# Kernel optimization log

Hardware: AMD Instinct MI355X
Metric: run time of the kernel (lower is better)

## Reference

```python
import jax, jax.numpy as jnp
import numpy as np
import math

N, L, C, H, K = 4, 16384, 256, 8, 4
D = C // H


def setup_inputs():
    rng = jax.random.key(0)
    ks = jax.random.split(rng, 16)
    def w(k, shape, scale):
        return jax.random.normal(k, shape, jnp.float32) * scale
    s = 1.0 / math.sqrt(C)
    return {
        "query": jax.random.normal(ks[0], (N, L, C), jnp.float32),
        "key": jax.random.normal(ks[1], (N, L, C), jnp.float32),
        "value": jax.random.normal(ks[2], (N, L, C), jnp.float32),
        "reference_points": jax.random.uniform(ks[3], (N, L, 2), jnp.float32),
        "pos_embed": jax.random.normal(ks[4], (N, L, C), jnp.float32),
        "Wq": w(ks[5], (C, C), s), "bq": jnp.zeros((C,), jnp.float32),
        "Wk": w(ks[6], (C, C), s), "bk": jnp.zeros((C,), jnp.float32),
        "Wv": w(ks[7], (C, C), s), "bv": jnp.zeros((C,), jnp.float32),
        "Wo1": w(ks[8], (C, 2 * C), s), "bo1": jnp.zeros((2 * C,), jnp.float32),
        "Wo2": w(ks[9], (2 * C, H * K * 2), 0.02), "bo2": w(ks[10], (H * K * 2,), 0.02),
        "Wpos": w(ks[11], (C, C), s), "bpos": jnp.zeros((C,), jnp.float32),
        "Wout": w(ks[12], (C, C), s), "bout": jnp.zeros((C,), jnp.float32),
    }


def _sample_weight(points):
    # F.grid_sample on a 1x1 feature map (bilinear, zeros padding, align_corners=False)
    # degenerates to a scalar weight: grid g = 2p-1, unnormalized c = g/2 = p - 0.5,
    # pixel-0 bilinear weight per axis = max(0, 1 - |c|).
    c = points - 0.5
    return jax.nn.relu(1.0 - jnp.abs(c[..., 0])) * jax.nn.relu(1.0 - jnp.abs(c[..., 1]))


def reference(query, key, value, reference_points, pos_embed,
              Wq, bq, Wk, bk, Wv, bv, Wo1, bo1, Wo2, bo2, Wpos, bpos, Wout, bout):
    Nb, Ln, Cd = query.shape
    q = (query @ Wq + bq).reshape(Nb, Ln, H, D)
    k = (key @ Wk + bk).reshape(Nb, Ln, H, D)
    v = (value @ Wv + bv).reshape(Nb, Ln, H, D)
    pos = (pos_embed @ Wpos + bpos).reshape(Nb, Ln, H, D)
    q = q + pos
    k = k + pos
    # offset MLP: Linear(C,2C) -> ReLU -> Linear(2C, H*K*2)
    offsets = (jax.nn.relu(query @ Wo1 + bo1) @ Wo2 + bo2).reshape(Nb, Ln, H, K, 2)
    sp = reference_points[:, :, None, None, :] + offsets  # [N,L,H,K,2]
    w = _sample_weight(sp)                                # [N,L,H,K]
    # sampled_k[n,l,h,k,:] = k[n,l,h,:] * w[n,l,h,k]  (1x1 grid_sample closed form)
    qk = jnp.einsum('nlhd,nlhd->nlh', q, k)               # [N,L,H]
    attn = jax.nn.softmax(qk[..., None] * w / math.sqrt(D), axis=-1)  # [N,L,H,K]
    # output = sum_k attn_k * (v * w_k) = v * sum_k(attn_k * w_k)
    wv = jnp.sum(attn * w, axis=-1)                       # [N,L,H]
    out = (v * wv[..., None]).reshape(Nb, Ln, Cd)
    return out @ Wout + bout
```

## Files before the change

### kernel.cpp

```cpp
#include <hip/hip_runtime.h>
#include <hip/hip_bf16.h>

typedef __bf16 bf16x8 __attribute__((ext_vector_type(8)));
typedef float f32x4 __attribute__((ext_vector_type(4)));
typedef float f32x2 __attribute__((ext_vector_type(2)));

#define MT 32
#define CC 256

__device__ __forceinline__ int swz(int r, int c) {
    return r * 512 + ((c * 2) ^ ((r & 7) << 4));
}
__device__ __forceinline__ int swzH(int r, int c) {
    return r * 1024 + ((c * 2) ^ ((r & 7) << 4));
}

__device__ __forceinline__ void zero4(f32x4 (&acc)[2][4]) {
#pragma unroll
    for (int i = 0; i < 2; ++i)
#pragma unroll
        for (int j = 0; j < 4; ++j)
            acc[i][j] = (f32x4){0.f, 0.f, 0.f, 0.f};
}

__device__ __forceinline__ void stage_load(const float* __restrict__ src, int row0, int tid,
                                           f32x4 (&v)[8]) {
#pragma unroll
    for (int i = 0; i < 8; ++i) {
        int f = i * 256 + tid;
        int r = f >> 6;
        int c = (f & 63) * 4;
        v[i] = __builtin_nontemporal_load((const f32x4*)(src + (size_t)(row0 + r) * CC + c));
    }
}
__device__ __forceinline__ void stage_write(__bf16* dst, int tid, const f32x4 (&v)[8]) {
#pragma unroll
    for (int i = 0; i < 8; ++i) {
        int f = i * 256 + tid;
        int r = f >> 6;
        int c = (f & 63) * 4;
        union { __bf16 h[4]; unsigned long long u; } uu;
        uu.h[0] = (__bf16)v[i][0]; uu.h[1] = (__bf16)v[i][1];
        uu.h[2] = (__bf16)v[i][2]; uu.h[3] = (__bf16)v[i][3];
        *(unsigned long long*)((char*)dst + swz(r, c)) = uu.u;
    }
}

__global__ void prep_all(const float* __restrict__ Wq, const float* __restrict__ Wk,
                         const float* __restrict__ Wpos, const float* __restrict__ Wo1,
                         const float* __restrict__ Wo2, const float* __restrict__ Wv,
                         const float* __restrict__ Wout, __bf16* __restrict__ ws)
{
    int i = blockIdx.x * 256 + threadIdx.x;
    if (i >= 557056) return;
    int j, K, N;
    const float* S0 = nullptr; const float* S1 = nullptr;
    if (i < 131072)      { j = i;          K = 512; N = 256; S0 = Wq;  S1 = Wpos; }
    else if (i < 262144) { j = i - 131072; K = 512; N = 256; S0 = Wk;  S1 = Wpos; }
    else if (i < 393216) { j = i - 262144; K = 256; N = 512; S0 = Wo1; }
    else if (i < 425984) { j = i - 393216; K = 512; N = 64;  S0 = Wo2; }
    else if (i < 491520) { j = i - 425984; K = 256; N = 256; S0 = Wv; }
    else                 { j = i - 491520; K = 256; N = 256; S0 = Wout; }
    int tile = j >> 9, r = j & 511;
    int lane = r >> 3, e = r & 7;
    int q4 = lane >> 4, r16 = lane & 15;
    int KC = K >> 5;
    int nc = tile / KC, kc = tile - nc * KC;
    int k = kc * 32 + q4 * 8 + e;
    int n = nc * 16 + r16;
    float v;
    if (S1 && k >= 256) v = S1[(size_t)(k - 256) * N + n];
    else                v = S0[(size_t)k * N + n];
    ws[i] = (__bf16)v;
}

extern "C" __global__ void __launch_bounds__(256, 2)
fused_ext_attn(const float* __restrict__ query, const float* __restrict__ key,
               const float* __restrict__ value, const float* __restrict__ refp,
               const float* __restrict__ pose,
               const __bf16* __restrict__ ws,
               const float* __restrict__ bq, const float* __restrict__ bk,
               const float* __restrict__ bv, const float* __restrict__ bpos,
               const float* __restrict__ bo1, const float* __restrict__ bo2,
               const float* __restrict__ bout,
               float* __restrict__ out)
{
    const __bf16* WTqp  = ws;
    const __bf16* WTkp  = ws + 131072;
    const __bf16* WTo1  = ws + 262144;
    const __bf16* WTo2  = ws + 393216;
    const __bf16* WTv   = ws + 425984;
    const __bf16* WTout = ws + 491520;

    __shared__ __attribute__((aligned(16))) __bf16 SA[MT * CC];
    __shared__ __attribute__((aligned(16))) __bf16 SB[MT * CC];
    __shared__ __attribute__((aligned(16))) __bf16 SC[MT * CC];
    __shared__ __attribute__((aligned(16))) char   H1[32768];

    float* off_s = (float*)H1;
    float* qk_s  = (float*)(H1 + 8192);
    float* wv_s  = (float*)(H1 + 9216);

    const int tid = threadIdx.x;
    const int lane = tid & 63;
    const int wid = tid >> 6;
    const int r16 = lane & 15;
    const int q4 = lane >> 4;
    const int laneoff = lane * 8;
    const int row0 = blockIdx.x * MT;

    f32x4 vq[8], vp[8], vkey[8];
    stage_load(query, row0, tid, vq);
    stage_load(pose, row0, tid, vp);
    stage_load(key, row0, tid, vkey);
    stage_write(SA, tid, vq);
    stage_write(SB, tid, vp);
    __syncthreads();

    stage_write(SC, tid, vkey);
    {
        f32x4 acc[2][8];
#pragma unroll
        for (int i = 0; i < 2; ++i)
#pragma unroll
            for (int j = 0; j < 8; ++j) acc[i][j] = (f32x4){0.f, 0.f, 0.f, 0.f};
#pragma unroll
        for (int ks = 0; ks < 8; ++ks) {
            int ak = ks * 32 + q4 * 8;
            bf16x8 a[2], b[8];
#pragma unroll
            for (int mf = 0; mf < 2; ++mf)
                a[mf] = *(const bf16x8*)((const char*)SA + swz(mf * 16 + r16, ak));
#pragma unroll
            for (int nf = 0; nf < 8; ++nf)
                b[nf] = *(const bf16x8*)(WTo1 + ((size_t)(wid * 8 + nf) * 8 + ks) * 512 + laneoff);
#pragma unroll
            for (int mf = 0; mf < 2; ++mf)
#pragma unroll
                for (int nf = 0; nf < 8; ++nf)
                    acc[mf][nf] = __builtin_amdgcn_mfma_f32_16x16x32_bf16(a[mf], b[nf], acc[mf][nf], 0, 0, 0);
        }
#pragma unroll
        for (int mf = 0; mf < 2; ++mf)
#pragma unroll
            for (int nf = 0; nf < 8; ++nf) {
                int col = wid * 128 + nf * 16 + r16;
                float bias = bo1[col];
#pragma unroll
                for (int r = 0; r < 4; ++r)
                    *(__bf16*)(H1 + swzH(mf * 16 + q4 * 4 + r, col)) =
                        (__bf16)fmaxf(acc[mf][nf][r] + bias, 0.f);
            }
    }
    __syncthreads();

    f32x4 accO[2];
    accO[0] = (f32x4){0.f, 0.f, 0.f, 0.f};
    accO[1] = (f32x4){0.f, 0.f, 0.f, 0.f};
#pragma unroll
    for (int ks = 0; ks < 16; ++ks) {
        int ak = ks * 32 + q4 * 8;
        bf16x8 b = *(const bf16x8*)(WTo2 + ((size_t)wid * 16 + ks) * 512 + laneoff);
#pragma unroll
        for (int mf = 0; mf < 2; ++mf) {
            bf16x8 a = *(const bf16x8*)(H1 + swzH(mf * 16 + r16, ak));
            accO[mf] = __builtin_amdgcn_mfma_f32_16x16x32_bf16(a, b, accO[mf], 0, 0, 0);
        }
    }
    __syncthreads();

    {
        int col = wid * 16 + r16;
        float b2 = bo2[col];
#pragma unroll
        for (int mf = 0; mf < 2; ++mf)
#pragma unroll
            for (int r = 0; r < 4; ++r)
                off_s[(mf * 16 + q4 * 4 + r) * 64 + col] = accO[mf][r] + b2;
    }
    f32x4 vval[8];
    stage_load(value, row0, tid, vval);
    {
        f32x4 qa[2][4], ka[2][4];
        zero4(qa); zero4(ka);
#pragma unroll
        for (int ks = 0; ks < 8; ++ks) {
            int ak = ks * 32 + q4 * 8;
            bf16x8 aq[2], akk[2];
#pragma unroll
            for (int mf = 0; mf < 2; ++mf) {
                aq[mf]  = *(const bf16x8*)((const char*)SA + swz(mf * 16 + r16, ak));
                akk[mf] = *(const bf16x8*)((const char*)SC + swz(mf * 16 + r16, ak));
            }
#pragma unroll
            for (int nf = 0; nf < 4; ++nf) {
                size_t toff = ((size_t)(wid * 4 + nf) * 16 + ks) * 512 + laneoff;
                bf16x8 bqf = *(const bf16x8*)(WTqp + toff);
                bf16x8 bkf = *(const bf16x8*)(WTkp + toff);
#pragma unroll
                for (int mf = 0; mf < 2; ++mf) {
                    qa[mf][nf] = __builtin_amdgcn_mfma_f32_16x16x32_bf16(aq[mf],  bqf, qa[mf][nf], 0, 0, 0);
                    ka[mf][nf] = __builtin_amdgcn_mfma_f32_16x16x32_bf16(akk[mf], bkf, ka[mf][nf], 0, 0, 0);
                }
            }
        }
#pragma unroll
        for (int ks = 8; ks < 16; ++ks) {
            int ak = (ks - 8) * 32 + q4 * 8;
            bf16x8 ap[2];
#pragma unroll
            for (int mf = 0; mf < 2; ++mf)
                ap[mf] = *(const bf16x8*)((const char*)SB + swz(mf * 16 + r16, ak));
#pragma unroll
            for (int nf = 0; nf < 4; ++nf) {
                size_t toff = ((size_t)(wid * 4 + nf) * 16 + ks) * 512 + laneoff;
                bf16x8 bqf = *(const bf16x8*)(WTqp + toff);
                bf16x8 bkf = *(const bf16x8*)(WTkp + toff);
#pragma unroll
                for (int mf = 0; mf < 2; ++mf) {
                    qa[mf][nf] = __builtin_amdgcn_mfma_f32_16x16x32_bf16(ap[mf], bqf, qa[mf][nf], 0, 0, 0);
                    ka[mf][nf] = __builtin_amdgcn_mfma_f32_16x16x32_bf16(ap[mf], bkf, ka[mf][nf], 0, 0, 0);
                }
            }
        }
        float Bq[4], Bk[4];
#pragma unroll
        for (int nf = 0; nf < 4; ++nf) {
            int col = wid * 64 + nf * 16 + r16;
            Bq[nf] = bq[col] + bpos[col];
            Bk[nf] = bk[col] + bpos[col];
        }
#pragma unroll
        for (int mf = 0; mf < 2; ++mf)
#pragma unroll
            for (int r = 0; r < 4; ++r) {
                float p0 = (qa[mf][0][r] + Bq[0]) * (ka[mf][0][r] + Bk[0])
                         + (qa[mf][1][r] + Bq[1]) * (ka[mf][1][r] + Bk[1]);
                float p1 = (qa[mf][2][r] + Bq[2]) * (ka[mf][2][r] + Bk[2])
                         + (qa[mf][3][r] + Bq[3]) * (ka[mf][3][r] + Bk[3]);
#pragma unroll
                for (int m = 1; m < 16; m <<= 1) {
                    p0 += __shfl_xor(p0, m);
                    p1 += __shfl_xor(p1, m);
                }
                if (r16 == 0) {
                    int row = mf * 16 + q4 * 4 + r;
                    f32x2 pq = {p0, p1};
                    *(f32x2*)&qk_s[row * 8 + wid * 2] = pq;
                }
            }
    }
    asm volatile("s_waitcnt lgkmcnt(0)" ::: "memory");
    __builtin_amdgcn_sched_barrier(0);
    {
        int t = lane >> 1, h = wid * 2 + (lane & 1);
        float qk = qk_s[t * 8 + h];
        f32x2 rp = __builtin_nontemporal_load((const f32x2*)(refp + (size_t)(row0 + t) * 2));
        float wgt[4], lg[4];
        float m = -1e30f;
#pragma unroll
        for (int kk = 0; kk < 4; ++kk) {
            float ox = off_s[t * 64 + (h * 4 + kk) * 2];
            float oy = off_s[t * 64 + (h * 4 + kk) * 2 + 1];
            float cx = rp[0] + ox - 0.5f, cy = rp[1] + oy - 0.5f;
            float wx = fmaxf(0.f, 1.f - fabsf(cx));
            float wy = fmaxf(0.f, 1.f - fabsf(cy));
            wgt[kk] = wx * wy;
            lg[kk] = qk * wgt[kk] * 0.17677669529663687f;
            m = fmaxf(m, lg[kk]);
        }
        float s = 0.f, sw = 0.f;
#pragma unroll
        for (int kk = 0; kk < 4; ++kk) {
            float e = __expf(lg[kk] - m);
            s += e;
            sw += e * wgt[kk];
        }
        wv_s[t * 8 + h] = sw / s;
    }
    __syncthreads();

    stage_write(SA, tid, vval);
    __syncthreads();

    {
        f32x4 acc[2][4];
        zero4(acc);
#pragma unroll
        for (int ks = 0; ks < 8; ++ks) {
            int ak = ks * 32 + q4 * 8;
            bf16x8 a[2], b[4];
#pragma unroll
            for (int mf = 0; mf < 2; ++mf)
                a[mf] = *(const bf16x8*)((const char*)SA + swz(mf * 16 + r16, ak));
#pragma unroll
            for (int nf = 0; nf < 4; ++nf)
                b[nf] = *(const bf16x8*)(WTv + ((size_t)(wid * 4 + nf) * 8 + ks) * 512 + laneoff);
#pragma unroll
            for (int mf = 0; mf < 2; ++mf)
#pragma unroll
                for (int nf = 0; nf < 4; ++nf)
                    acc[mf][nf] = __builtin_amdgcn_mfma_f32_16x16x32_bf16(a[mf], b[nf], acc[mf][nf], 0, 0, 0);
        }
#pragma unroll
        for (int mf = 0; mf < 2; ++mf)
#pragma unroll
            for (int nf = 0; nf < 4; ++nf) {
                int col = wid * 64 + nf * 16 + r16;
                float bias = bv[col];
#pragma unroll
                for (int r = 0; r < 4; ++r) {
                    int row = mf * 16 + q4 * 4 + r;
                    float wvv = wv_s[row * 8 + (col >> 5)];
                    *(__bf16*)((char*)SC + swz(row, col)) = (__bf16)((acc[mf][nf][r] + bias) * wvv);
                }
            }
    }
    __syncthreads();

    {
        f32x4 acc[2][4];
        zero4(acc);
#pragma unroll
        for (int ks = 0; ks < 8; ++ks) {
            int ak = ks * 32 + q4 * 8;
            bf16x8 a[2], b[4];
#pragma unroll
            for (int mf = 0; mf < 2; ++mf)
                a[mf] = *(const bf16x8*)((const char*)SC + swz(mf * 16 + r16, ak));
#pragma unroll
            for (int nf = 0; nf < 4; ++nf)
                b[nf] = *(const bf16x8*)(WTout + ((size_t)(wid * 4 + nf) * 8 + ks) * 512 + laneoff);
#pragma unroll
            for (int mf = 0; mf < 2; ++mf)
#pragma unroll
                for (int nf = 0; nf < 4; ++nf)
                    acc[mf][nf] = __builtin_amdgcn_mfma_f32_16x16x32_bf16(a[mf], b[nf], acc[mf][nf], 0, 0, 0);
        }
#pragma unroll
        for (int mf = 0; mf < 2; ++mf)
#pragma unroll
            for (int nf = 0; nf < 4; ++nf) {
                int col = wid * 64 + nf * 16 + r16;
                float bias = bout[col];
#pragma unroll
                for (int r = 0; r < 4; ++r) {
                    int row = mf * 16 + q4 * 4 + r;
                    __builtin_nontemporal_store(acc[mf][nf][r] + bias,
                                                out + (size_t)(row0 + row) * CC + col);
                }
            }
    }
}

extern "C" void kernel_launch(void* const* d_in, const int* in_sizes, int n_in,
                              void* d_out, int out_size, void* d_ws, size_t ws_size,
                              hipStream_t stream)
{
    const float* query = (const float*)d_in[0];
    const float* key   = (const float*)d_in[1];
    const float* value = (const float*)d_in[2];
    const float* refp  = (const float*)d_in[3];
    const float* pose  = (const float*)d_in[4];
    const float* Wq  = (const float*)d_in[5];  const float* bq   = (const float*)d_in[6];
    const float* Wk  = (const float*)d_in[7];  const float* bk   = (const float*)d_in[8];
    const float* Wv  = (const float*)d_in[9];  const float* bv   = (const float*)d_in[10];
    const float* Wo1 = (const float*)d_in[11]; const float* bo1  = (const float*)d_in[12];
    const float* Wo2 = (const float*)d_in[13]; const float* bo2  = (const float*)d_in[14];
    const float* Wpos= (const float*)d_in[15]; const float* bpos = (const float*)d_in[16];
    const float* Wout= (const float*)d_in[17]; const float* bout = (const float*)d_in[18];

    __bf16* ws = (__bf16*)d_ws;

    prep_all<<<2176, 256, 0, stream>>>(Wq, Wk, Wpos, Wo1, Wo2, Wv, Wout, ws);

    fused_ext_attn<<<65536 / MT, 256, 0, stream>>>(
        query, key, value, refp, pose, ws,
        bq, bk, bv, bpos, bo1, bo2, bout, (float*)d_out);
}
```

Measured before the change: 150.5 us.

## Use 512-thread blocks, splitting each GEMM's columns across eight waves

Result: faster. 146.8 us (-2.5%).

```diff
diff --git a/kernel.cpp b/kernel.cpp
--- a/kernel.cpp
+++ b/kernel.cpp
@@ -15,28 +15,20 @@
     return r * 1024 + ((c * 2) ^ ((r & 7) << 4));
 }
 
-__device__ __forceinline__ void zero4(f32x4 (&acc)[2][4]) {
-#pragma unroll
-    for (int i = 0; i < 2; ++i)
-#pragma unroll
-        for (int j = 0; j < 4; ++j)
-            acc[i][j] = (f32x4){0.f, 0.f, 0.f, 0.f};
-}
-
 __device__ __forceinline__ void stage_load(const float* __restrict__ src, int row0, int tid,
-                                           f32x4 (&v)[8]) {
-#pragma unroll
-    for (int i = 0; i < 8; ++i) {
-        int f = i * 256 + tid;
+                                           f32x4 (&v)[4]) {
+#pragma unroll
+    for (int i = 0; i < 4; ++i) {
+        int f = i * 512 + tid;
         int r = f >> 6;
         int c = (f & 63) * 4;
         v[i] = __builtin_nontemporal_load((const f32x4*)(src + (size_t)(row0 + r) * CC + c));
     }
 }
-__device__ __forceinline__ void stage_write(__bf16* dst, int tid, const f32x4 (&v)[8]) {
-#pragma unroll
-    for (int i = 0; i < 8; ++i) {
-        int f = i * 256 + tid;
+__device__ __forceinline__ void stage_write(__bf16* dst, int tid, const f32x4 (&v)[4]) {
+#pragma unroll
+    for (int i = 0; i < 4; ++i) {
+        int f = i * 512 + tid;
         int r = f >> 6;
         int c = (f & 63) * 4;
         union { __bf16 h[4]; unsigned long long u; } uu;
@@ -74,7 +66,7 @@
     ws[i] = (__bf16)v;
 }
 
-extern "C" __global__ void __launch_bounds__(256, 2)
+extern "C" __global__ void __launch_bounds__(512, 4)
 fused_ext_attn(const float* __restrict__ query, const float* __restrict__ key,
                const float* __restrict__ value, const float* __restrict__ refp,
                const float* __restrict__ pose,
@@ -109,7 +101,7 @@
     const int laneoff = lane * 8;
     const int row0 = blockIdx.x * MT;
 
-    f32x4 vq[8], vp[8], vkey[8];
+    f32x4 vq[4], vp[4], vkey[4];
     stage_load(query, row0, tid, vq);
     stage_load(pose, row0, tid, vp);
     stage_load(key, row0, tid, vkey);
@@ -119,32 +111,32 @@
 
     stage_write(SC, tid, vkey);
     {
-        f32x4 acc[2][8];
+        f32x4 acc[2][4];
 #pragma unroll
         for (int i = 0; i < 2; ++i)
 #pragma unroll
-            for (int j = 0; j < 8; ++j) acc[i][j] = (f32x4){0.f, 0.f, 0.f, 0.f};
+            for (int j = 0; j < 4; ++j) acc[i][j] = (f32x4){0.f, 0.f, 0.f, 0.f};
 #pragma unroll
         for (int ks = 0; ks < 8; ++ks) {
             int ak = ks * 32 + q4 * 8;
-            bf16x8 a[2], b[8];
+            bf16x8 a[2], b[4];
 #pragma unroll
             for (int mf = 0; mf < 2; ++mf)
                 a[mf] = *(const bf16x8*)((const char*)SA + swz(mf * 16 + r16, ak));
 #pragma unroll
-            for (int nf = 0; nf < 8; ++nf)
-                b[nf] = *(const bf16x8*)(WTo1 + ((size_t)(wid * 8 + nf) * 8 + ks) * 512 + laneoff);
-#pragma unroll
-            for (int mf = 0; mf < 2; ++mf)
-#pragma unroll
-                for (int nf = 0; nf < 8; ++nf)
+            for (int nf = 0; nf < 4; ++nf)
+                b[nf] = *(const bf16x8*)(WTo1 + ((size_t)(wid * 4 + nf) * 8 + ks) * 512 + laneoff);
+#pragma unroll
+            for (int mf = 0; mf < 2; ++mf)
+#pragma unroll
+                for (int nf = 0; nf < 4; ++nf)
                     acc[mf][nf] = __builtin_amdgcn_mfma_f32_16x16x32_bf16(a[mf], b[nf], acc[mf][nf], 0, 0, 0);
         }
 #pragma unroll
         for (int mf = 0; mf < 2; ++mf)
 #pragma unroll
-            for (int nf = 0; nf < 8; ++nf) {
-                int col = wid * 128 + nf * 16 + r16;
+            for (int nf = 0; nf < 4; ++nf) {
+                int col = wid * 64 + nf * 16 + r16;
                 float bias = bo1[col];
 #pragma unroll
                 for (int r = 0; r < 4; ++r)
@@ -157,32 +149,30 @@
     f32x4 accO[2];
     accO[0] = (f32x4){0.f, 0.f, 0.f, 0.f};
     accO[1] = (f32x4){0.f, 0.f, 0.f, 0.f};
-#pragma unroll
-    for (int ks = 0; ks < 16; ++ks) {
-        int ak = ks * 32 + q4 * 8;
-        bf16x8 b = *(const bf16x8*)(WTo2 + ((size_t)wid * 16 + ks) * 512 + laneoff);
-#pragma unroll
-        for (int mf = 0; mf < 2; ++mf) {
-            bf16x8 a = *(const bf16x8*)(H1 + swzH(mf * 16 + r16, ak));
-            accO[mf] = __builtin_amdgcn_mfma_f32_16x16x32_bf16(a, b, accO[mf], 0, 0, 0);
-        }
-    }
-    __syncthreads();
-
+    if (wid < 4) {
+#pragma unroll
+        for (int ks = 0; ks < 16; ++ks) {
+            int ak = ks * 32 + q4 * 8;
+            bf16x8 b = *(const bf16x8*)(WTo2 + ((size_t)wid * 16 + ks) * 512 + laneoff);
+#pragma unroll
+            for (int mf = 0; mf < 2; ++mf) {
+                bf16x8 a = *(const bf16x8*)(H1 + swzH(mf * 16 + r16, ak));
+                accO[mf] = __builtin_amdgcn_mfma_f32_16x16x32_bf16(a, b, accO[mf], 0, 0, 0);
+            }
+        }
+    }
+    f32x4 vval[4];
+    stage_load(value, row0, tid, vval);
+    float qk_r[2][4];
     {
-        int col = wid * 16 + r16;
-        float b2 = bo2[col];
-#pragma unroll
-        for (int mf = 0; mf < 2; ++mf)
-#pragma unroll
-            for (int r = 0; r < 4; ++r)
-                off_s[(mf * 16 + q4 * 4 + r) * 64 + col] = accO[mf][r] + b2;
-    }
-    f32x4 vval[8];
-    stage_load(value, row0, tid, vval);
-    {
-        f32x4 qa[2][4], ka[2][4];
-        zero4(qa); zero4(ka);
+        f32x4 qa[2][2], ka[2][2];
+#pragma unroll
+        for (int i = 0; i < 2; ++i)
+#pragma unroll
+            for (int j = 0; j < 2; ++j) {
+                qa[i][j] = (f32x4){0.f, 0.f, 0.f, 0.f};
+                ka[i][j] = (f32x4){0.f, 0.f, 0.f, 0.f};
+            }
 #pragma unroll
         for (int ks = 0; ks < 8; ++ks) {
             int ak = ks * 32 + q4 * 8;
@@ -193,8 +183,8 @@
                 akk[mf] = *(const bf16x8*)((const char*)SC + swz(mf * 16 + r16, ak));
             }
 #pragma unroll
-            for (int nf = 0; nf < 4; ++nf) {
-                size_t toff = ((size_t)(wid * 4 + nf) * 16 + ks) * 512 + laneoff;
+            for (int nf = 0; nf < 2; ++nf) {
+                size_t toff = ((size_t)(wid * 2 + nf) * 16 + ks) * 512 + laneoff;
                 bf16x8 bqf = *(const bf16x8*)(WTqp + toff);
                 bf16x8 bkf = *(const bf16x8*)(WTkp + toff);
 #pragma unroll
@@ -212,8 +202,8 @@
             for (int mf = 0; mf < 2; ++mf)
                 ap[mf] = *(const bf16x8*)((const char*)SB + swz(mf * 16 + r16, ak));
 #pragma unroll
-            for (int nf = 0; nf < 4; ++nf) {
-                size_t toff = ((size_t)(wid * 4 + nf) * 16 + ks) * 512 + laneoff;
+            for (int nf = 0; nf < 2; ++nf) {
+                size_t toff = ((size_t)(wid * 2 + nf) * 16 + ks) * 512 + laneoff;
                 bf16x8 bqf = *(const bf16x8*)(WTqp + toff);
                 bf16x8 bkf = *(const bf16x8*)(WTkp + toff);
 #pragma unroll
@@ -223,10 +213,10 @@
                 }
             }
         }
-        float Bq[4], Bk[4];
-#pragma unroll
-        for (int nf = 0; nf < 4; ++nf) {
-            int col = wid * 64 + nf * 16 + r16;
+        float Bq[2], Bk[2];
+#pragma unroll
+        for (int nf = 0; nf < 2; ++nf) {
+            int col = wid * 32 + nf * 16 + r16;
             Bq[nf] = bq[col] + bpos[col];
             Bk[nf] = bk[col] + bpos[col];
         }
@@ -236,24 +226,35 @@
             for (int r = 0; r < 4; ++r) {
                 float p0 = (qa[mf][0][r] + Bq[0]) * (ka[mf][0][r] + Bk[0])
                          + (qa[mf][1][r] + Bq[1]) * (ka[mf][1][r] + Bk[1]);
-                float p1 = (qa[mf][2][r] + Bq[2]) * (ka[mf][2][r] + Bk[2])
-                         + (qa[mf][3][r] + Bq[3]) * (ka[mf][3][r] + Bk[3]);
-#pragma unroll
-                for (int m = 1; m < 16; m <<= 1) {
+#pragma unroll
+                for (int m = 1; m < 16; m <<= 1)
                     p0 += __shfl_xor(p0, m);
-                    p1 += __shfl_xor(p1, m);
-                }
-                if (r16 == 0) {
-                    int row = mf * 16 + q4 * 4 + r;
-                    f32x2 pq = {p0, p1};
-                    *(f32x2*)&qk_s[row * 8 + wid * 2] = pq;
-                }
-            }
-    }
-    asm volatile("s_waitcnt lgkmcnt(0)" ::: "memory");
-    __builtin_amdgcn_sched_barrier(0);
-    {
-        int t = lane >> 1, h = wid * 2 + (lane & 1);
+                qk_r[mf][r] = p0;
+            }
+    }
+    __syncthreads();
+
+    stage_write(SA, tid, vval);
+    if (wid < 4) {
+        int col = wid * 16 + r16;
+        float b2 = bo2[col];
+#pragma unroll
+        for (int mf = 0; mf < 2; ++mf)
+#pragma unroll
+            for (int r = 0; r < 4; ++r)
+                off_s[(mf * 16 + q4 * 4 + r) * 64 + col] = accO[mf][r] + b2;
+    }
+    if (r16 == 0) {
+#pragma unroll
+        for (int mf = 0; mf < 2; ++mf)
+#pragma unroll
+            for (int r = 0; r < 4; ++r)
+                qk_s[(mf * 16 + q4 * 4 + r) * 8 + wid] = qk_r[mf][r];
+    }
+    __syncthreads();
+
+    if (tid < 256) {
+        int t = tid >> 3, h = tid & 7;
         float qk = qk_s[t * 8 + h];
         f32x2 rp = __builtin_nontemporal_load((const f32x2*)(refp + (size_t)(row0 + t) * 2));
         float wgt[4], lg[4];
@@ -280,38 +281,38 @@
     }
     __syncthreads();
 
-    stage_write(SA, tid, vval);
-    __syncthreads();
-
     {
-        f32x4 acc[2][4];
-        zero4(acc);
+        f32x4 acc[2][2];
+#pragma unroll
+        for (int i = 0; i < 2; ++i)
+#pragma unroll
+            for (int j = 0; j < 2; ++j) acc[i][j] = (f32x4){0.f, 0.f, 0.f, 0.f};
 #pragma unroll
         for (int ks = 0; ks < 8; ++ks) {
             int ak = ks * 32 + q4 * 8;
-            bf16x8 a[2], b[4];
+            bf16x8 a[2], b[2];
 #pragma unroll
             for (int mf = 0; mf < 2; ++mf)
                 a[mf] = *(const bf16x8*)((const char*)SA + swz(mf * 16 + r16, ak));
 #pragma unroll
-            for (int nf = 0; nf < 4; ++nf)
-                b[nf] = *(const bf16x8*)(WTv + ((size_t)(wid * 4 + nf) * 8 + ks) * 512 + laneoff);
-#pragma unroll
-            for (int mf = 0; mf < 2; ++mf)
-#pragma unroll
-                for (int nf = 0; nf < 4; ++nf)
+            for (int nf = 0; nf < 2; ++nf)
+                b[nf] = *(const bf16x8*)(WTv + ((size_t)(wid * 2 + nf) * 8 + ks) * 512 + laneoff);
+#pragma unroll
+            for (int mf = 0; mf < 2; ++mf)
+#pragma unroll
+                for (int nf = 0; nf < 2; ++nf)
                     acc[mf][nf] = __builtin_amdgcn_mfma_f32_16x16x32_bf16(a[mf], b[nf], acc[mf][nf], 0, 0, 0);
         }
 #pragma unroll
         for (int mf = 0; mf < 2; ++mf)
 #pragma unroll
-            for (int nf = 0; nf < 4; ++nf) {
-                int col = wid * 64 + nf * 16 + r16;
+            for (int nf = 0; nf < 2; ++nf) {
+                int col = wid * 32 + nf * 16 + r16;
                 float bias = bv[col];
 #pragma unroll
                 for (int r = 0; r < 4; ++r) {
                     int row = mf * 16 + q4 * 4 + r;
-                    float wvv = wv_s[row * 8 + (col >> 5)];
+                    float wvv = wv_s[row * 8 + wid];
                     *(__bf16*)((char*)SC + swz(row, col)) = (__bf16)((acc[mf][nf][r] + bias) * wvv);
                 }
             }
@@ -319,29 +320,32 @@
     __syncthreads();
 
     {
-        f32x4 acc[2][4];
-        zero4(acc);
+        f32x4 acc[2][2];
+#pragma unroll
+        for (int i = 0; i < 2; ++i)
+#pragma unroll
+            for (int j = 0; j < 2; ++j) acc[i][j] = (f32x4){0.f, 0.f, 0.f, 0.f};
 #pragma unroll
         for (int ks = 0; ks < 8; ++ks) {
             int ak = ks * 32 + q4 * 8;
-            bf16x8 a[2], b[4];
+            bf16x8 a[2], b[2];
 #pragma unroll
             for (int mf = 0; mf < 2; ++mf)
                 a[mf] = *(const bf16x8*)((const char*)SC + swz(mf * 16 + r16, ak));
 #pragma unroll
-            for (int nf = 0; nf < 4; ++nf)
-                b[nf] = *(const bf16x8*)(WTout + ((size_t)(wid * 4 + nf) * 8 + ks) * 512 + laneoff);
-#pragma unroll
-            for (int mf = 0; mf < 2; ++mf)
-#pragma unroll
-                for (int nf = 0; nf < 4; ++nf)
+            for (int nf = 0; nf < 2; ++nf)
+                b[nf] = *(const bf16x8*)(WTout + ((size_t)(wid * 2 + nf) * 8 + ks) * 512 + laneoff);
+#pragma unroll
+            for (int mf = 0; mf < 2; ++mf)
+#pragma unroll
+                for (int nf = 0; nf < 2; ++nf)
                     acc[mf][nf] = __builtin_amdgcn_mfma_f32_16x16x32_bf16(a[mf], b[nf], acc[mf][nf], 0, 0, 0);
         }
 #pragma unroll
         for (int mf = 0; mf < 2; ++mf)
 #pragma unroll
-            for (int nf = 0; nf < 4; ++nf) {
-                int col = wid * 64 + nf * 16 + r16;
+            for (int nf = 0; nf < 2; ++nf) {
+                int col = wid * 32 + nf * 16 + r16;
                 float bias = bout[col];
 #pragma unroll
                 for (int r = 0; r < 4; ++r) {
@@ -374,7 +378,7 @@
 
     prep_all<<<2176, 256, 0, stream>>>(Wq, Wk, Wpos, Wo1, Wo2, Wv, Wout, ws);
 
-    fused_ext_attn<<<65536 / MT, 256, 0, stream>>>(
+    fused_ext_attn<<<65536 / MT, 512, 0, stream>>>(
         query, key, value, refp, pose, ws,
         bq, bk, bv, bpos, bo1, bo2, bout, (float*)d_out);
 }
```
